# Kernel tuning notes

Hardware: AMD Instinct MI355X
Metric: run time of the kernel (lower is better)

## Reference

```python
import jax, jax.numpy as jnp
import numpy as np

N_HEADS = 16
CONTEXT_WINDOW = 256


def _band_mask(s_q, s_k):
    # True = masked out. Module (causal=True, context_window=256) allows only
    # keys with 0 <= (query_pos - key_pos) < CONTEXT_WINDOW (causal mask is
    # subsumed by the lower band).
    d = jnp.arange(s_q)[:, None] - jnp.arange(s_k)[None, :]
    return ~((d >= 0) & (d < CONTEXT_WINDOW))


def setup_inputs() -> dict:
    key = jax.random.key(0)
    ks = jax.random.split(key, 5)
    B, S, D = 2, 2048, 1024
    std = 0.02
    return {
        "query": jax.random.normal(ks[0], (B, S, D), dtype=jnp.float32),
        "Wq": jax.random.normal(ks[1], (D, D), dtype=jnp.float32) * std,
        "bq": jnp.zeros((D,), dtype=jnp.float32),
        "Wk": jax.random.normal(ks[2], (D, D), dtype=jnp.float32) * std,
        "bk": jnp.zeros((D,), dtype=jnp.float32),
        "Wv": jax.random.normal(ks[3], (D, D), dtype=jnp.float32) * std,
        "bv": jnp.zeros((D,), dtype=jnp.float32),
        "Wo": jax.random.normal(ks[4], (D, D), dtype=jnp.float32) * std,
        "bo": jnp.zeros((D,), dtype=jnp.float32),
    }


def reference(query, Wq, bq, Wk, bk, Wv, bv, Wo, bo):
    B, S, D = query.shape
    H = N_HEADS
    Dh = D // H
    # projections -> [B, H, S, Dh]
    q = (query @ Wq + bq).reshape(B, S, H, Dh).transpose(0, 2, 1, 3)
    k = (query @ Wk + bk).reshape(B, S, H, Dh).transpose(0, 2, 1, 3)
    v = (query @ Wv + bv).reshape(B, S, H, Dh).transpose(0, 2, 1, 3)
    scores = jnp.einsum("bhqd,bhkd->bhqk", q, k) * (1.0 / np.sqrt(Dh))
    mask = _band_mask(S, S)  # [S, S]
    scores = jnp.where(mask[None, None, :, :], -jnp.inf, scores)
    attn = jax.nn.softmax(scores, axis=-1)
    out = jnp.einsum("bhqk,bhkd->bhqd", attn, v)
    out = out.transpose(0, 2, 1, 3).reshape(B, S, D)
    return out @ Wo + bo
```

## Files before the change

kernel.cpp:

```cpp
#include <hip/hip_runtime.h>
#include <hip/hip_bf16.h>


typedef __bf16 bf16x8 __attribute__((ext_vector_type(8)));
typedef float f32x4 __attribute__((ext_vector_type(4)));
typedef short s16x4 __attribute__((ext_vector_type(4)));
typedef unsigned short u16x8 __attribute__((ext_vector_type(8)));
typedef unsigned short u16x4 __attribute__((ext_vector_type(4)));

__device__ __forceinline__ unsigned short f2bf(float f) {
  unsigned int u = __builtin_bit_cast(unsigned int, f);
  u += 0x7FFFu + ((u >> 16) & 1u);
  return (unsigned short)(u >> 16);
}

__device__ __forceinline__ f32x4 mfma32(bf16x8 a, bf16x8 b, f32x4 c) {
  return __builtin_amdgcn_mfma_f32_16x16x32_bf16(a, b, c, 0, 0, 0);
}
__device__ __forceinline__ f32x4 mfma16(s16x4 a, s16x4 b, f32x4 c) {
  return __builtin_amdgcn_mfma_f32_16x16x16bf16_1k(a, b, c, 0, 0, 0);
}

__device__ __forceinline__ void gl16(const unsigned short* gsrc,
                                     unsigned short* lds) {
  __builtin_amdgcn_global_load_lds(
      (const __attribute__((address_space(1))) unsigned int*)gsrc,
      (__attribute__((address_space(3))) unsigned int*)lds, 16, 0, 0);
}

__global__ __launch_bounds__(256) void cvt_x(const float* __restrict__ x,
                                             unsigned short* __restrict__ xb) {
  const int i = blockIdx.x * 256 + threadIdx.x;
  const float4 v = ((const float4*)x)[i];
  u16x4 o = { f2bf(v.x), f2bf(v.y), f2bf(v.z), f2bf(v.w) };
  *(u16x4*)(xb + (size_t)i * 4) = o;
}

__global__ __launch_bounds__(256) void cvt_w(const float* __restrict__ Wq,
                                             const float* __restrict__ Wk,
                                             const float* __restrict__ Wv,
                                             const float* __restrict__ Wo,
                                             unsigned short* __restrict__ Wt) {
  const int z = blockIdx.z;
  const float* W = (z == 0) ? Wq : (z == 1) ? Wk : (z == 2) ? Wv : Wo;
  unsigned short* dst = Wt + (size_t)z * 1024 * 1024;
  __shared__ float t[32][33];
  const int x = threadIdx.x, y = threadIdx.y;
  const int n0 = blockIdx.x * 32, k0 = blockIdx.y * 32;
#pragma unroll
  for (int i = 0; i < 32; i += 8)
    t[y + i][x] = W[(size_t)(k0 + y + i) * 1024 + n0 + x];
  __syncthreads();
#pragma unroll
  for (int i = 0; i < 32; i += 8)
    dst[(size_t)(n0 + y + i) * 1024 + k0 + x] = f2bf(t[x][y + i]);
}

template <int BN, int MODE>
__global__ __launch_bounds__(256) void gemm_lds(
    const unsigned short* __restrict__ A, const unsigned short* __restrict__ Bt,
    const float* __restrict__ bq, const float* __restrict__ bk,
    const float* __restrict__ bv,
    unsigned short* __restrict__ q_ws, unsigned short* __restrict__ k_ws,
    unsigned short* __restrict__ v_ws,
    const float* __restrict__ bo, float* __restrict__ outp) {
  constexpr int ACC_N = BN / 32;
  __shared__ unsigned short Alds[128 * 32];
  __shared__ unsigned short Blds[BN * 32];
  const int tid = threadIdx.x, lane = tid & 63, w = tid >> 6;
  const int lq = lane & 15, lg = lane >> 4;
  const int bm = blockIdx.x, bn = blockIdx.y;
  const int wr = (w >> 1) * 64, wc = (w & 1) * (BN / 2);

  const int srow = lane >> 2, scol8 = (lane & 3) * 8;
  const unsigned short* Ag =
      A + (size_t)(bm * 128 + w * 32 + srow) * 1024 + scol8;
  const unsigned short* Bg =
      (BN == 128) ? Bt + (size_t)(bn * 128 + w * 32 + srow) * 1024 + scol8
                  : Bt + (size_t)(bn * 64 + w * 16 + srow) * 1024 + scol8;
  unsigned short* Al0 = Alds + (w * 32) * 32;
  unsigned short* Al1 = Alds + (w * 32 + 16) * 32;
  unsigned short* Bl0 = (BN == 128) ? Blds + (w * 32) * 32
                                    : Blds + (w * 16) * 32;
  unsigned short* Bl1 = Blds + (w * 32 + 16) * 32;

  f32x4 acc[4][ACC_N] = {};
  for (int kt = 0; kt < 1024; kt += 32) {
    __syncthreads();
    gl16(Ag + kt, Al0);
    gl16(Ag + kt + 16 * 1024, Al1);
    gl16(Bg + kt, Bl0);
    if (BN == 128) gl16(Bg + kt + 16 * 1024, Bl1);
    __syncthreads();
    bf16x8 af[4], bfr[ACC_N];
#pragma unroll
    for (int m = 0; m < 4; ++m)
      af[m] = *(const bf16x8*)(Alds + (wr + m * 16 + lq) * 32 + lg * 8);
#pragma unroll
    for (int n = 0; n < ACC_N; ++n)
      bfr[n] = *(const bf16x8*)(Blds + (wc + n * 16 + lq) * 32 + lg * 8);
#pragma unroll
    for (int m = 0; m < 4; ++m)
#pragma unroll
      for (int n = 0; n < ACC_N; ++n)
        acc[m][n] = mfma32(af[m], bfr[n], acc[m][n]);
  }

  const int r0 = bm * 128 + wr + lg * 4;
  const int c0g = bn * BN + wc + lq;
#pragma unroll
  for (int m = 0; m < 4; ++m) {
#pragma unroll
    for (int n = 0; n < ACC_N; ++n) {
      const int col = c0g + n * 16;
#pragma unroll
      for (int j = 0; j < 4; ++j) {
        const int row = r0 + m * 16 + j;
        float v = acc[m][n][j];
        if (MODE == 0) {
          const int t = col >> 10, cc = col & 1023;
          const float* bias = (t == 0) ? bq : ((t == 1) ? bk : bv);
          v += bias[cc];
          if (t == 0) v *= 0.125f;
          unsigned short* dst = (t == 0) ? q_ws : ((t == 1) ? k_ws : v_ws);
          const int h = cc >> 6, dh = cc & 63, b = row >> 11, s = row & 2047;
          dst[((size_t)(b * 16 + h) * 2048 + s) * 64 + dh] = f2bf(v);
        } else {
          outp[(size_t)row * 1024 + col] = v + bo[col];
        }
      }
    }
  }
}

__global__ __launch_bounds__(256) void attn_kernel(
    const unsigned short* __restrict__ q_ws,
    const unsigned short* __restrict__ k_ws,
    const unsigned short* __restrict__ v_ws,
    unsigned short* __restrict__ attn_out) {
  __shared__ unsigned short o_lds[4][16 * 64];
  const int tid = threadIdx.x, lane = tid & 63, w = tid >> 6;
  const int lq = lane & 15, lg = lane >> 4;
  const int bh = blockIdx.y;
  const int q0 = blockIdx.x * 64 + w * 16;
  const unsigned short* Q = q_ws + (size_t)bh * 2048 * 64;
  const unsigned short* Kp = k_ws + (size_t)bh * 2048 * 64;
  const unsigned short* Vp = v_ws + (size_t)bh * 2048 * 64;

  const bf16x8 qf0 = *(const bf16x8*)(Q + (size_t)(q0 + lq) * 64 + lg * 8);
  const bf16x8 qf1 = *(const bf16x8*)(Q + (size_t)(q0 + lq) * 64 + 32 + lg * 8);

  float m = -1e30f, lsum = 0.f;
  f32x4 oacc[4] = {};
  int t0 = (q0 - 255) >> 4;
  if (t0 < 0) t0 = 0;
  const int t1 = q0 >> 4;

  for (int t = t0; t <= t1; ++t) {
    const int j0 = t * 16;
    const bf16x8 kf0 = *(const bf16x8*)(Kp + (size_t)(j0 + lq) * 64 + lg * 8);
    const bf16x8 kf1 =
        *(const bf16x8*)(Kp + (size_t)(j0 + lq) * 64 + 32 + lg * 8);
    f32x4 st = {};
    st = mfma32(kf0, qf0, st);
    st = mfma32(kf1, qf1, st);

    float s[4], p[4];
    bool ok[4];
#pragma unroll
    for (int r = 0; r < 4; ++r) {
      const int delta = (q0 + lq) - (j0 + lg * 4 + r);
      ok[r] = (delta >= 0) && (delta < 256);
      s[r] = ok[r] ? st[r] : -1e30f;
    }
    float mt = fmaxf(fmaxf(s[0], s[1]), fmaxf(s[2], s[3]));
    mt = fmaxf(mt, __shfl_xor(mt, 16));
    mt = fmaxf(mt, __shfl_xor(mt, 32));
    const float mn = fmaxf(m, mt);
    const float scale = __expf(m - mn);
    float ps = 0.f;
#pragma unroll
    for (int r = 0; r < 4; ++r) {
      p[r] = ok[r] ? __expf(s[r] - mn) : 0.f;
      ps += p[r];
    }
    ps += __shfl_xor(ps, 16);
    ps += __shfl_xor(ps, 32);
    lsum = lsum * scale + ps;
    m = mn;
#pragma unroll
    for (int c = 0; c < 4; ++c)
#pragma unroll
      for (int r = 0; r < 4; ++r) oacc[c][r] *= scale;

    s16x4 pb = { (short)f2bf(p[0]), (short)f2bf(p[1]),
                 (short)f2bf(p[2]), (short)f2bf(p[3]) };
#pragma unroll
    for (int c = 0; c < 4; ++c) {
      s16x4 vf;
#pragma unroll
      for (int j = 0; j < 4; ++j)
        vf[j] = (short)Vp[(size_t)(j0 + lg * 4 + j) * 64 + c * 16 + lq];
      oacc[c] = mfma16(vf, pb, oacc[c]);
    }
  }

  const float rl = 1.f / lsum;
#pragma unroll
  for (int c = 0; c < 4; ++c)
#pragma unroll
    for (int r = 0; r < 4; ++r)
      o_lds[w][lq * 64 + c * 16 + lg * 4 + r] = f2bf(oacc[c][r] * rl);
  __syncthreads();
  const int row = lane >> 2, d0 = (lane & 3) * 16;
  const u16x8 o0 = *(const u16x8*)(&o_lds[w][row * 64 + d0]);
  const u16x8 o1 = *(const u16x8*)(&o_lds[w][row * 64 + d0 + 8]);
  const size_t g =
      ((size_t)((bh >> 4) * 2048 + q0 + row)) * 1024 + (bh & 15) * 64 + d0;
  *(u16x8*)(attn_out + g) = o0;
  *(u16x8*)(attn_out + g + 8) = o1;
}

extern "C" void kernel_launch(void* const* d_in, const int* in_sizes, int n_in,
                              void* d_out, int out_size, void* d_ws,
                              size_t ws_size, hipStream_t stream) {
  const float* query = (const float*)d_in[0];
  const float* Wq = (const float*)d_in[1];
  const float* bq = (const float*)d_in[2];
  const float* Wk = (const float*)d_in[3];
  const float* bk = (const float*)d_in[4];
  const float* Wv = (const float*)d_in[5];
  const float* bv = (const float*)d_in[6];
  const float* Wo = (const float*)d_in[7];
  const float* bo = (const float*)d_in[8];
  float* outp = (float*)d_out;

  char* ws = (char*)d_ws;
  unsigned short* xbf = (unsigned short*)(ws);
  unsigned short* wt  = (unsigned short*)(ws + (8u << 20));
  unsigned short* qws = (unsigned short*)(ws + (16u << 20));
  unsigned short* kws = (unsigned short*)(ws + (24u << 20));
  unsigned short* vws = (unsigned short*)(ws + (32u << 20));

  cvt_x<<<4096, 256, 0, stream>>>(query, xbf);
  cvt_w<<<dim3(32, 32, 4), dim3(32, 8), 0, stream>>>(Wq, Wk, Wv, Wo, wt);
  gemm_lds<128, 0><<<dim3(32, 24), 256, 0, stream>>>(
      xbf, wt, bq, bk, bv, qws, kws, vws, nullptr, nullptr);
  attn_kernel<<<dim3(32, 32), 256, 0, stream>>>(qws, kws, vws, xbf);
  gemm_lds<64, 1><<<dim3(32, 16), 256, 0, stream>>>(
      xbf, wt + (size_t)3 * 1024 * 1024, nullptr, nullptr, nullptr, nullptr,
      nullptr, nullptr, bo, outp);
}
```

Baseline: 98.07 us.

## Double GEMM K-tile depth and remap workgroups across XCDs for cache locality

```diff
diff --git a/kernel.cpp b/kernel.cpp
--- a/kernel.cpp
+++ b/kernel.cpp
@@ -65,45 +65,54 @@
     unsigned short* __restrict__ v_ws,
     const float* __restrict__ bo, float* __restrict__ outp) {
   constexpr int ACC_N = BN / 32;
-  __shared__ unsigned short Alds[128 * 32];
-  __shared__ unsigned short Blds[BN * 32];
+  __shared__ unsigned short Alds[128 * 64];
+  __shared__ unsigned short Blds[BN * 64];
   const int tid = threadIdx.x, lane = tid & 63, w = tid >> 6;
   const int lq = lane & 15, lg = lane >> 4;
-  const int bm = blockIdx.x, bn = blockIdx.y;
+
+  const int nwgx = gridDim.x;
+  const int hw = blockIdx.x + blockIdx.y * nwgx;
+  const int cpx = (nwgx * gridDim.y) >> 3;
+  const int logical = (hw & 7) * cpx + (hw >> 3);
+  const int bm = logical % nwgx, bn = logical / nwgx;
+
   const int wr = (w >> 1) * 64, wc = (w & 1) * (BN / 2);
 
-  const int srow = lane >> 2, scol8 = (lane & 3) * 8;
+  const int srow8 = lane >> 3, scol8 = (lane & 7) * 8;
   const unsigned short* Ag =
-      A + (size_t)(bm * 128 + w * 32 + srow) * 1024 + scol8;
+      A + (size_t)(bm * 128 + w * 32 + srow8) * 1024 + scol8;
   const unsigned short* Bg =
-      (BN == 128) ? Bt + (size_t)(bn * 128 + w * 32 + srow) * 1024 + scol8
-                  : Bt + (size_t)(bn * 64 + w * 16 + srow) * 1024 + scol8;
-  unsigned short* Al0 = Alds + (w * 32) * 32;
-  unsigned short* Al1 = Alds + (w * 32 + 16) * 32;
-  unsigned short* Bl0 = (BN == 128) ? Blds + (w * 32) * 32
-                                    : Blds + (w * 16) * 32;
-  unsigned short* Bl1 = Blds + (w * 32 + 16) * 32;
+      Bt + (size_t)(bn * BN + w * (BN / 4) + srow8) * 1024 + scol8;
+  unsigned short* AlW = Alds + (w * 32) * 64;
+  unsigned short* BlW = Blds + (w * (BN / 4)) * 64;
 
   f32x4 acc[4][ACC_N] = {};
-  for (int kt = 0; kt < 1024; kt += 32) {
+  for (int kt = 0; kt < 1024; kt += 64) {
     __syncthreads();
-    gl16(Ag + kt, Al0);
-    gl16(Ag + kt + 16 * 1024, Al1);
-    gl16(Bg + kt, Bl0);
-    if (BN == 128) gl16(Bg + kt + 16 * 1024, Bl1);
+#pragma unroll
+    for (int i = 0; i < 4; ++i)
+      gl16(Ag + kt + (size_t)i * 8 * 1024, AlW + i * 8 * 64);
+#pragma unroll
+    for (int i = 0; i < BN / 32; ++i)
+      gl16(Bg + kt + (size_t)i * 8 * 1024, BlW + i * 8 * 64);
     __syncthreads();
-    bf16x8 af[4], bfr[ACC_N];
-#pragma unroll
-    for (int m = 0; m < 4; ++m)
-      af[m] = *(const bf16x8*)(Alds + (wr + m * 16 + lq) * 32 + lg * 8);
-#pragma unroll
-    for (int n = 0; n < ACC_N; ++n)
-      bfr[n] = *(const bf16x8*)(Blds + (wc + n * 16 + lq) * 32 + lg * 8);
-#pragma unroll
-    for (int m = 0; m < 4; ++m)
+#pragma unroll
+    for (int kk = 0; kk < 2; ++kk) {
+      bf16x8 af[4], bfr[ACC_N];
+#pragma unroll
+      for (int m = 0; m < 4; ++m)
+        af[m] =
+            *(const bf16x8*)(Alds + (wr + m * 16 + lq) * 64 + kk * 32 + lg * 8);
 #pragma unroll
       for (int n = 0; n < ACC_N; ++n)
-        acc[m][n] = mfma32(af[m], bfr[n], acc[m][n]);
+        bfr[n] =
+            *(const bf16x8*)(Blds + (wc + n * 16 + lq) * 64 + kk * 32 + lg * 8);
+#pragma unroll
+      for (int m = 0; m < 4; ++m)
+#pragma unroll
+        for (int n = 0; n < ACC_N; ++n)
+          acc[m][n] = mfma32(af[m], bfr[n], acc[m][n]);
+    }
   }
 
   const int r0 = bm * 128 + wr + lg * 4;
@@ -141,8 +150,12 @@
   __shared__ unsigned short o_lds[4][16 * 64];
   const int tid = threadIdx.x, lane = tid & 63, w = tid >> 6;
   const int lq = lane & 15, lg = lane >> 4;
-  const int bh = blockIdx.y;
-  const int q0 = blockIdx.x * 64 + w * 16;
+
+  const int hw = blockIdx.x + (blockIdx.y << 5);
+  const int logical = (hw & 7) * 128 + (hw >> 3);
+  const int bx = logical & 31, bh = logical >> 5;
+
+  const int q0 = bx * 64 + w * 16;
   const unsigned short* Q = q_ws + (size_t)bh * 2048 * 64;
   const unsigned short* Kp = k_ws + (size_t)bh * 2048 * 64;
   const unsigned short* Vp = v_ws + (size_t)bh * 2048 * 64;
```

After: 122.5 us. 1.25x slower.

## Double-buffer LDS tiles in projection GEMM to overlap loads with MFMA

Applied to the files above, without the earlier changes.

```diff
diff --git a/kernel.cpp b/kernel.cpp
--- a/kernel.cpp
+++ b/kernel.cpp
@@ -65,8 +65,8 @@
     unsigned short* __restrict__ v_ws,
     const float* __restrict__ bo, float* __restrict__ outp) {
   constexpr int ACC_N = BN / 32;
-  __shared__ unsigned short Alds[128 * 32];
-  __shared__ unsigned short Blds[BN * 32];
+  __shared__ unsigned short Alds[2][128 * 32];
+  __shared__ unsigned short Blds[2][BN * 32];
   const int tid = threadIdx.x, lane = tid & 63, w = tid >> 6;
   const int lq = lane & 15, lg = lane >> 4;
   const int bm = blockIdx.x, bn = blockIdx.y;
@@ -78,32 +78,38 @@
   const unsigned short* Bg =
       (BN == 128) ? Bt + (size_t)(bn * 128 + w * 32 + srow) * 1024 + scol8
                   : Bt + (size_t)(bn * 64 + w * 16 + srow) * 1024 + scol8;
-  unsigned short* Al0 = Alds + (w * 32) * 32;
-  unsigned short* Al1 = Alds + (w * 32 + 16) * 32;
-  unsigned short* Bl0 = (BN == 128) ? Blds + (w * 32) * 32
-                                    : Blds + (w * 16) * 32;
-  unsigned short* Bl1 = Blds + (w * 32 + 16) * 32;
+  const int aOffW = (w * 32) * 32, aOffW1 = (w * 32 + 16) * 32;
+  const int bOffW = (BN == 128) ? (w * 32) * 32 : (w * 16) * 32;
+  const int bOffW1 = (w * 32 + 16) * 32;
+
+  auto stage = [&](int kt, int buf) {
+    gl16(Ag + kt, &Alds[buf][aOffW]);
+    gl16(Ag + kt + 16 * 1024, &Alds[buf][aOffW1]);
+    gl16(Bg + kt, &Blds[buf][bOffW]);
+    if (BN == 128) gl16(Bg + kt + 16 * 1024, &Blds[buf][bOffW1]);
+  };
+
+  stage(0, 0);
+  __syncthreads();
 
   f32x4 acc[4][ACC_N] = {};
+  int cur = 0;
   for (int kt = 0; kt < 1024; kt += 32) {
-    __syncthreads();
-    gl16(Ag + kt, Al0);
-    gl16(Ag + kt + 16 * 1024, Al1);
-    gl16(Bg + kt, Bl0);
-    if (BN == 128) gl16(Bg + kt + 16 * 1024, Bl1);
-    __syncthreads();
+    if (kt < 1024 - 32) stage(kt + 32, cur ^ 1);
     bf16x8 af[4], bfr[ACC_N];
 #pragma unroll
     for (int m = 0; m < 4; ++m)
-      af[m] = *(const bf16x8*)(Alds + (wr + m * 16 + lq) * 32 + lg * 8);
+      af[m] = *(const bf16x8*)(&Alds[cur][(wr + m * 16 + lq) * 32 + lg * 8]);
 #pragma unroll
     for (int n = 0; n < ACC_N; ++n)
-      bfr[n] = *(const bf16x8*)(Blds + (wc + n * 16 + lq) * 32 + lg * 8);
+      bfr[n] = *(const bf16x8*)(&Blds[cur][(wc + n * 16 + lq) * 32 + lg * 8]);
 #pragma unroll
     for (int m = 0; m < 4; ++m)
 #pragma unroll
       for (int n = 0; n < ACC_N; ++n)
         acc[m][n] = mfma32(af[m], bfr[n], acc[m][n]);
+    __syncthreads();
+    cur ^= 1;
   }
 
   const int r0 = bm * 128 + wr + lg * 4;
```

After: 102.5 us. 1.04x slower.
